# Kernel tuning notes

Hardware: AMD Instinct MI355X
Metric: run time of the kernel (lower is better)

Reference implementation:

```python
import jax, jax.numpy as jnp
import numpy as np
from jax import lax

B, LATENT, HC, COND_OUT, H, INPUT = 64, 512, 1024, 512, 1024, 389
S, SEQ = 16, 512
NOTES = SEQ // S  # 32 notes per subsequence
NL = 2


def _lstm_cell(x, h, c, Wih, Whh, bih, bhh):
    # PyTorch LSTM cell, gate order i, f, g, o
    g = x @ Wih.T + h @ Whh.T + bih + bhh
    i, f, gg, o = jnp.split(g, 4, axis=-1)
    c_new = jax.nn.sigmoid(f) * c + jax.nn.sigmoid(i) * jnp.tanh(gg)
    h_new = jax.nn.sigmoid(o) * jnp.tanh(c_new)
    return h_new, c_new


def setup_inputs() -> dict:
    key = jax.random.key(0)
    ks = iter(jax.random.split(key, 32))
    s = 0.03  # ~ PyTorch LSTM uniform(-1/sqrt(H), 1/sqrt(H)) scale
    def W(shape):
        return jax.random.normal(next(ks), shape, jnp.float32) * s
    return {
        "latent": jax.random.normal(next(ks), (B, LATENT), jnp.float32),
        "target": jax.random.randint(next(ks), (B, SEQ), 0, INPUT),
        "teacher_forcing": 0,
        "h0_dec": jax.random.normal(next(ks), (S, NL, B, H), jnp.float32),
        "c0_dec": jax.random.normal(next(ks), (S, NL, B, H), jnp.float32),
        # conductor LSTM (2 layers)
        "Wih_c0": W((4 * HC, LATENT)), "Whh_c0": W((4 * HC, HC)),
        "bih_c0": W((4 * HC,)), "bhh_c0": W((4 * HC,)),
        "Wih_c1": W((4 * HC, HC)), "Whh_c1": W((4 * HC, HC)),
        "bih_c1": W((4 * HC,)), "bhh_c1": W((4 * HC,)),
        # conductor output projection
        "Wco": W((COND_OUT, HC)), "bco": W((COND_OUT,)),
        # decoder LSTM (2 layers); input = concat(prev_note, emb) -> INPUT+COND_OUT
        "Wih_d0": W((4 * H, INPUT + COND_OUT)), "Whh_d0": W((4 * H, H)),
        "bih_d0": W((4 * H,)), "bhh_d0": W((4 * H,)),
        "Wih_d1": W((4 * H, H)), "Whh_d1": W((4 * H, H)),
        "bih_d1": W((4 * H,)), "bhh_d1": W((4 * H,)),
        # decoder output projection
        "Wdo": W((INPUT, H)), "bdo": W((INPUT,)),
    }


def reference(latent, target, teacher_forcing, h0_dec, c0_dec,
              Wih_c0, Whh_c0, bih_c0, bhh_c0, Wih_c1, Whh_c1, bih_c1, bhh_c1,
              Wco, bco,
              Wih_d0, Whh_d0, bih_d0, bhh_d0, Wih_d1, Whh_d1, bih_d1, bhh_d1,
              Wdo, bdo):
    # use_teacher_forcing is hard-coded False in the source; target is unused.
    del target, teacher_forcing

    def outer(carry, xs):
        hc, cc, prev = carry          # hc, cc: [2,B,HC]; prev: [B,INPUT]
        hd_init, cd_init = xs         # [2,B,H] random decoder init per subsequence
        h0, c0 = _lstm_cell(latent, hc[0], cc[0], Wih_c0, Whh_c0, bih_c0, bhh_c0)
        h1, c1 = _lstm_cell(h0, hc[1], cc[1], Wih_c1, Whh_c1, bih_c1, bhh_c1)
        emb = jnp.tanh(h1 @ Wco.T + bco)  # [B, COND_OUT]

        def inner(ic, _):
            p, hdi, cdi = ic
            x = jnp.concatenate([p, emb], axis=-1)  # [B, INPUT+COND_OUT]
            hd0, cd0 = _lstm_cell(x, hdi[0], cdi[0], Wih_d0, Whh_d0, bih_d0, bhh_d0)
            hd1, cd1 = _lstm_cell(hd0, hdi[1], cdi[1], Wih_d1, Whh_d1, bih_d1, bhh_d1)
            note = jnp.tanh(hd1 @ Wdo.T + bdo)  # [B, INPUT]
            return (note, jnp.stack([hd0, hd1]), jnp.stack([cd0, cd1])), note

        (prev_new, _, _), notes = lax.scan(inner, (prev, hd_init, cd_init), None, length=NOTES)
        return (jnp.stack([h0, h1]), jnp.stack([c0, c1]), prev_new), notes

    init = (jnp.zeros((NL, B, HC), jnp.float32),
            jnp.zeros((NL, B, HC), jnp.float32),
            jnp.zeros((B, INPUT), jnp.float32))
    _, out = lax.scan(outer, init, (h0_dec, c0_dec))
    # out: [S, NOTES, B, INPUT] -> [B, SEQ, INPUT]
    return out.transpose(2, 0, 1, 3).reshape(B, SEQ, INPUT)
```

## Files before the change

### kernel.cpp

```cpp
#include <hip/hip_runtime.h>
#include <hip/hip_bf16.h>

typedef unsigned int  u32;
typedef unsigned short u16;
typedef __attribute__((ext_vector_type(8))) short short8;
typedef __attribute__((ext_vector_type(4))) float f32x4;
typedef __attribute__((ext_vector_type(4))) unsigned int u32x4;
typedef __attribute__((ext_vector_type(2))) unsigned int u32x2;

#define MFMA(a,b,c) __builtin_amdgcn_mfma_f32_16x16x32_bf16(a,b,c,0,0,0)

#define NWG    256
#define KD0    1448
#define KD1    2056
#define KPROJ  1032

#define WS_ARR   0
#define WS_DONE  1024
#define WS_SEM   1536
#define SEM_HD0  0
#define SEM_HD1  1
#define SEM_NOTE 2
#define SEM_I0   3
#define SEM_I1   4

#define WS_NOTE  4096
#define WS_HD0   (WS_NOTE + 2*52*64*8*2)
#define WS_HD1   (WS_HD0 + 2*128*64*8*2)
#define WS_HC0   (WS_HD1 + 2*128*64*8*2)
#define WS_HC1   (WS_HC0 + 2*128*64*8*2)
#define WS_EMB   (WS_HC1 + 2*128*64*8*2)
#define WS_LAT   (WS_EMB + 15*64*64*8*2)
#define WS_END   (WS_EMB + 16*64*64*8*2)

#define NOTE_PAR 26624
#define HD_PAR   65536
#define HC_PAR   65536
#define EMB_S    32768

#define L_GSC   0
#define L_GC0X  8448
#define L_CC0   12800
#define L_CC1   13824
#define L_BC1   14848
#define L_PACK  14912
#define L_ROLE  16960
#define L_WD0   L_ROLE
#define L_G0E   (L_ROLE + 32*KD0*2)
#define L_CST0  (L_G0E + 8448)
#define L_BD0   (L_CST0 + 2048)
#define L_WPJ   (L_BD0 + 128)
#define L_BPJ   (L_WPJ + 16*KPROJ*2)
#define L_WD1   L_ROLE
#define L_CST1  (L_ROLE + 32*KD1*2)
#define L_BD1   (L_CST1 + 2048)
#define LDS_BYTES 153600

__device__ __forceinline__ u16 f2bf(float f){
  u32 u = __float_as_uint(f);
  u32 r = (u + 0x7FFFu + ((u >> 16) & 1u)) >> 16;
  return (u16)r;
}
__device__ __forceinline__ float sigm(float x){ return 1.f/(1.f + __expf(-x)); }
__device__ __forceinline__ float tanh_(float x){
  float e = __expf(-2.f*fabsf(x));
  float t = (1.f - e)/(1.f + e);
  return x < 0.f ? -t : t;
}
__device__ __forceinline__ short8 ldw8(const float* p0){
  short8 r;
#pragma unroll
  for (int j = 0; j < 8; ++j) r[j] = (short)f2bf(p0[j]);
  return r;
}

__device__ __forceinline__ void gst1(u32* p, u32 v){
  asm volatile("global_store_dword %0, %1, off sc1" :: "v"(p), "v"(v) : "memory");
}
__device__ __forceinline__ void gst4(u16* p, u32x4 v){
  asm volatile("global_store_dwordx4 %0, %1, off sc1" :: "v"(p), "v"(v) : "memory");
}
__device__ __forceinline__ u32 ld1_sc1(const u32* p){
  u32 v;
  asm volatile("global_load_dword %0, %1, off sc1\n\ts_waitcnt vmcnt(0)"
               : "=v"(v) : "v"(p) : "memory");
  return v;
}

#define AISSUE(dst, addr) \
  asm volatile("global_load_dwordx4 %0, %1, off sc1" : "=&v"(dst) : "v"(addr) : "memory")
#define AWAITN(cnt) do{ \
  asm volatile("s_waitcnt vmcnt(" #cnt ")" ::: "memory"); \
  __builtin_amdgcn_sched_barrier(0x3F7); }while(0)

template<int NA, int NB, bool TWO>
__device__ __forceinline__ void mm_lds(
    const u16* Wl, int ldw16, const u16* xal, const u16* xbl,
    f32x4& a0, f32x4& a1)
{
  constexpr int N = NA + NB;
  constexpr int R = (N < 32) ? N : 32;
  short8 ab[R];
#define XADDR(i) (((i) < NA) ? (xal + (size_t)(i)*2048) : (xbl + (size_t)((i)-NA)*2048))
#define ACONS(i) { \
    a0 = MFMA(ab[(i) % R], *(const short8*)(Wl + (size_t)(i)*32), a0); \
    if constexpr (TWO) a1 = MFMA(ab[(i) % R], *(const short8*)(Wl + ldw16 + (size_t)(i)*32), a1); }
  if constexpr (N <= 32){
#pragma unroll
    for (int i = 0; i < N; ++i) AISSUE(ab[i], XADDR(i));
    AWAITN(0);
#pragma unroll
    for (int i = 0; i < N; ++i) ACONS(i);
  } else {
#pragma unroll
    for (int i = 0; i < 32; ++i) AISSUE(ab[i], XADDR(i));
#pragma unroll
    for (int i = 0; i < N - 32; ++i){
      AWAITN(31);
      ACONS(i);
      AISSUE(ab[i & 31], XADDR(i + 32));
    }
    AWAITN(0);
#pragma unroll
    for (int i = N - 32; i < N; ++i) ACONS(i);
  }
#undef ACONS
#undef XADDR
}

template<int NA, int NB, bool TWO>
__device__ __forceinline__ void mm_gw(
    const float* w00, const float* w01, const float* w10, const float* w11,
    const u16* xal, const u16* xbl, f32x4& a0, f32x4& a1)
{
  constexpr int N = NA + NB;
  static_assert((N % 16) == 0, "");
  short8 ab[16];
#define XADDR(i) (((i) < NA) ? (xal + (size_t)(i)*2048) : (xbl + (size_t)((i)-NA)*2048))
#pragma unroll
  for (int b = 0; b < N/16; ++b){
#pragma unroll
    for (int j = 0; j < 16; ++j) AISSUE(ab[j], XADDR(b*16 + j));
    AWAITN(0);
#pragma unroll
    for (int j = 0; j < 16; ++j){
      const int i = b*16 + j;
      const float* wp0 = (i < NA) ? (w00 + (size_t)i*32) : (w01 + (size_t)(i-NA)*32);
      a0 = MFMA(ab[j], ldw8(wp0), a0);
      if constexpr (TWO){
        const float* wp1 = (i < NA) ? (w10 + (size_t)i*32) : (w11 + (size_t)(i-NA)*32);
        a1 = MFMA(ab[j], ldw8(wp1), a1);
      }
    }
  }
#undef XADDR
}

__device__ __forceinline__ void sem_post_lane(char* ws, int sem, int wg){
  asm volatile("s_waitcnt vmcnt(0)" ::: "memory");
  if (threadIdx.x == 0){
    u32* c = (u32*)(ws + WS_SEM + sem*512 + (wg & 7)*64);
    __hip_atomic_fetch_add(c, 1u, __ATOMIC_RELAXED, __HIP_MEMORY_SCOPE_AGENT);
  }
}
__device__ __forceinline__ void sem_wait(char* ws, int sem, u32 target){
  if (threadIdx.x < 64){
    const int l = threadIdx.x;
    const u32* c = (const u32*)(ws + WS_SEM + sem*512 + l*64);
    for (;;){
      u32 v = (l < 8) ? ld1_sc1(c) : 0u;
#pragma unroll
      for (int off = 32; off; off >>= 1)
        v += (u32)__shfl_xor((int)v, off, 64);
      if (v >= target) break;
      __builtin_amdgcn_s_sleep(1);
    }
  }
  __syncthreads();
}

__device__ __forceinline__ void gbar(char* ws, int grp, int mem, u32 ep){
  u32* arr  = (u32*)(ws + WS_ARR) + grp*32;
  u32* done = (u32*)(ws + WS_DONE);
  asm volatile("s_waitcnt vmcnt(0)" ::: "memory");
  __syncthreads();
  if (threadIdx.x < 64){
    const int l = threadIdx.x;
    if (l == 0) gst1(&arr[mem], ep);
    if (mem == 0){
      for (;;){
        u32 m = (l < 32) ? ld1_sc1(&arr[l]) : ep;
#pragma unroll
        for (int off = 32; off; off >>= 1){
          u32 o = (u32)__shfl_xor((int)m, off, 64);
          m = o < m ? o : m;
        }
        if (m >= ep) break;
      }
      if (l == 0) gst1(&done[grp], ep);
    }
    for (;;){
      u32 m = (l < 8) ? ld1_sc1(&done[l]) : ep;
#pragma unroll
      for (int off = 32; off; off >>= 1){
        u32 o = (u32)__shfl_xor((int)m, off, 64);
        m = o < m ? o : m;
      }
      if (m >= ep) break;
      __builtin_amdgcn_s_sleep(1);
    }
  }
  __syncthreads();
}

struct Params {
  const float *latent, *h0_dec, *c0_dec;
  const float *Wih_c0, *Whh_c0, *bih_c0, *bhh_c0;
  const float *Wih_c1, *Whh_c1, *bih_c1, *bhh_c1;
  const float *Wco, *bco;
  const float *Wih_d0, *Whh_d0, *bih_d0, *bhh_d0;
  const float *Wih_d1, *Whh_d1, *bih_d1, *bhh_d1;
  const float *Wdo, *bdo;
  float* out;
  char* ws;
};

__device__ __forceinline__ void cell_pw(
    const float* g_sc, const float* gadd, const float* bias,
    float* cst, u32* pack, int tid)
{
  const int b = tid & 63, k = tid >> 6;
  u32 hp = 0;
#pragma unroll
  for (int j = 0; j < 2; ++j){
    const int u = 2*k + j;
    float gi = g_sc[b*33 + u];
    float gf = g_sc[b*33 + 8 + u];
    float gg = g_sc[b*33 + 16 + u];
    float go = g_sc[b*33 + 24 + u];
    if (gadd){
      gi += gadd[b*33 + u];      gf += gadd[b*33 + 8 + u];
      gg += gadd[b*33 + 16 + u]; go += gadd[b*33 + 24 + u];
    }
    if (bias){
      gi += bias[u]; gf += bias[8 + u]; gg += bias[16 + u]; go += bias[24 + u];
    }
    float c = sigm(gf)*cst[u*64 + b] + sigm(gi)*tanh_(gg);
    const float h = sigm(go)*tanh_(c);
    cst[u*64 + b] = c;
    hp |= ((u32)f2bf(h)) << (16*j);
  }
  pack[b*4 + k] = hp;
}

__device__ __forceinline__ void cond_pw(
    f32x4 acc, const float* gadd17, const float* bias16,
    float* cstL, u16* pack16, int lane, int wid)
{
  const int r = lane & 15, q = lane >> 4, m0 = wid*16;
  float v[4], vf[4], vg[4], vo[4];
#pragma unroll
  for (int i = 0; i < 4; ++i){
    const int brow = m0 + q*4 + i;
    float x = acc[i];
    if (gadd17) x += gadd17[brow*17 + r];
    if (bias16) x += bias16[r];
    v[i] = x;
  }
#pragma unroll
  for (int i = 0; i < 4; ++i){
    vf[i] = __shfl_xor(v[i], 4, 64);
    vg[i] = __shfl_xor(v[i], 8, 64);
    vo[i] = __shfl_xor(v[i], 12, 64);
  }
  if (r < 4){
#pragma unroll
    for (int i = 0; i < 4; ++i){
      const int brow = m0 + q*4 + i;
      float c = sigm(vf[i])*cstL[r*64 + brow] + sigm(v[i])*tanh_(vg[i]);
      const float h = sigm(vo[i])*tanh_(c);
      cstL[r*64 + brow] = c;
      pack16[brow*4 + r] = f2bf(h);
    }
  }
}

__global__ void init_kernel(const float* latent, char* ws){
  const int i = blockIdx.x*blockDim.x + threadIdx.x;
  if (i < 1024) ((u32*)ws)[i] = 0u;
  if (i < 26624) ((u32*)(ws + WS_NOTE))[i] = 0u;
  if (i < 65536){ ((u32*)(ws + WS_HC0))[i] = 0u; ((u32*)(ws + WS_HC1))[i] = 0u; }
  if (i < 32768){
    const int b = i >> 9, k = i & 511;
    ((u16*)(ws + WS_LAT))[((size_t)(k >> 3)*64 + b)*8 + (k & 7)] = f2bf(latent[i]);
  }
}

__global__ void __launch_bounds__(256, 1) decoder_kernel(Params P){
  extern __shared__ char smem[];
  const int wg = blockIdx.x, tid = threadIdx.x;
  const int lane = tid & 63, wid = tid >> 6;
  const int rr = lane & 15, q = lane >> 4, m0 = wid*16;
  const int grp = wg >> 5, mem = wg & 31;

  u16* noteb = (u16*)(P.ws + WS_NOTE);
  u16* hd0b  = (u16*)(P.ws + WS_HD0);
  u16* hd1b  = (u16*)(P.ws + WS_HD1);
  u16* hc0b  = (u16*)(P.ws + WS_HC0);
  u16* hc1b  = (u16*)(P.ws + WS_HC1);
  u16* embA  = (u16*)(P.ws + WS_EMB);
  const u16* latg = (const u16*)(P.ws + WS_LAT);

  float* g_sc  = (float*)(smem + L_GSC);
  float* g_c0x = (float*)(smem + L_GC0X);
  float* cc0   = (float*)(smem + L_CC0);
  float* cc1   = (float*)(smem + L_CC1);
  float* bc1   = (float*)(smem + L_BC1);
  u16*   pack16 = (u16*)(smem + L_PACK);
  u32*   packU32 = (u32*)(smem + L_PACK);
  u16*   Wd0  = (u16*)(smem + L_WD0);
  float* g0e  = (float*)(smem + L_G0E);
  float* cst0 = (float*)(smem + L_CST0);
  float* bd0  = (float*)(smem + L_BD0);
  u16*   Wpj  = (u16*)(smem + L_WPJ);
  float* bpj  = (float*)(smem + L_BPJ);
  u16*   Wd1  = (u16*)(smem + L_WD1);
  float* cst1 = (float*)(smem + L_CST1);
  float* bd1  = (float*)(smem + L_BD1);

  const bool is_d0 = (wg < 128);
  const int lofs = (q*64 + m0 + rr)*8;

  if (is_d0){
    for (int r = wid; r < 32; r += 4){
      const int grow = ((r >> 3) << 10) + 8*wg + (r & 7);
      const float* wih = P.Wih_d0 + (size_t)grow*901;
      const float* whh = P.Whh_d0 + (size_t)grow*1024;
      u16* dst = Wd0 + (size_t)r*KD0;
      for (int c = lane; c < 416; c += 64) dst[c] = (c < 389) ? f2bf(wih[c]) : (u16)0;
      for (int c = lane; c < 1024; c += 64) dst[416 + c] = f2bf(whh[c]);
    }
    if (tid < 32){
      const int grow = ((tid >> 3) << 10) + 8*wg + (tid & 7);
      bd0[tid] = P.bih_d0[grow] + P.bhh_d0[grow];
    }
    if (wg < 25){
      for (int r = wid; r < 16; r += 4){
        const int row = 16*wg + r;
        u16* dst = Wpj + (size_t)r*KPROJ;
        if (row < 389){
          const float* w = P.Wdo + (size_t)row*1024;
          for (int c = lane; c < 1024; c += 64) dst[c] = f2bf(w[c]);
        } else {
          for (int c = lane; c < 1024; c += 64) dst[c] = 0;
        }
      }
      if (tid < 16){
        const int row = 16*wg + tid;
        bpj[tid] = (row < 389) ? P.bdo[row] : 0.f;
      }
    }
  } else {
    const int wl = wg - 128;
    for (int r = wid; r < 32; r += 4){
      const int grow = ((r >> 3) << 10) + 8*wl + (r & 7);
      const float* wih = P.Wih_d1 + (size_t)grow*1024;
      const float* whh = P.Whh_d1 + (size_t)grow*1024;
      u16* dst = Wd1 + (size_t)r*KD1;
      for (int c = lane; c < 1024; c += 64) dst[c] = f2bf(wih[c]);
      for (int c = lane; c < 1024; c += 64) dst[1024 + c] = f2bf(whh[c]);
    }
    if (tid < 32){
      const int grow = ((tid >> 3) << 10) + 8*wl + (tid & 7);
      bd1[tid] = P.bih_d1[grow] + P.bhh_d1[grow];
    }
  }
  if (tid < 256){ cc0[tid] = 0.f; cc1[tid] = 0.f; }
  if (tid < 16){
    const int grow = ((tid >> 2) << 10) + 4*wg + (tid & 3);
    bc1[tid] = P.bih_c1[grow] + P.bhh_c1[grow];
  }
  {
    const int grow = ((rr >> 2) << 10) + 4*wg + (rr & 3);
    f32x4 acc = {0.f,0.f,0.f,0.f}, dummy;
    mm_gw<16,0,false>(P.Wih_c0 + (size_t)grow*512 + q*8, nullptr, nullptr, nullptr,
                      latg + lofs, latg + lofs, acc, dummy);
    const float bias = P.bih_c0[grow] + P.bhh_c0[grow];
#pragma unroll
    for (int i = 0; i < 4; ++i)
      g_c0x[(m0 + q*4 + i)*17 + rr] = acc[i] + bias;
  }
  __syncthreads();

  u32 ep = 0;
#define GBAR() gbar(P.ws, grp, mem, ++ep)

  for (int s = 0; s < 16; ++s){
    const int pc = s & 1;
    const u16* hc0_p = hc0b + (size_t)pc*HC_PAR;
    u16*       hc0_n = hc0b + (size_t)(pc ^ 1)*HC_PAR;
    const u16* hc1_p = hc1b + (size_t)pc*HC_PAR;
    u16*       hc1_n = hc1b + (size_t)(pc ^ 1)*HC_PAR;
    const int grow = ((rr >> 2) << 10) + 4*wg + (rr & 3);

    {
      f32x4 acc = {0.f,0.f,0.f,0.f}, dummy;
      mm_gw<32,0,false>(P.Whh_c0 + (size_t)grow*1024 + q*8, nullptr, nullptr, nullptr,
                        hc0_p + lofs, hc0_p + lofs, acc, dummy);
      cond_pw(acc, g_c0x, nullptr, cc0, pack16, lane, wid);
    }
    __syncthreads();
    if (tid < 64){
      u32x2 v = *(const u32x2*)&packU32[tid*2];
      asm volatile("global_store_dwordx2 %0, %1, off sc1"
                   :: "v"(hc0_n + ((size_t)(wg >> 1)*64 + tid)*8 + (wg & 1)*4), "v"(v) : "memory");
    }
    GBAR();

    {
      f32x4 acc = {0.f,0.f,0.f,0.f}, dummy;
      mm_gw<32,32,false>(P.Wih_c1 + (size_t)grow*1024 + q*8,
                         P.Whh_c1 + (size_t)grow*1024 + q*8, nullptr, nullptr,
                         hc0_n + lofs, hc1_p + lofs, acc, dummy);
      cond_pw(acc, nullptr, bc1, cc1, pack16, lane, wid);
    }
    __syncthreads();
    if (tid < 64){
      u32x2 v = *(const u32x2*)&packU32[tid*2];
      asm volatile("global_store_dwordx2 %0, %1, off sc1"
                   :: "v"(hc1_n + ((size_t)(wg >> 1)*64 + tid)*8 + (wg & 1)*4), "v"(v) : "memory");
    }
    GBAR();

    if (wg < 32){
      const int row = 16*wg + rr;
      f32x4 acc = {0.f,0.f,0.f,0.f}, dummy;
      mm_gw<32,0,false>(P.Wco + (size_t)row*1024 + q*8, nullptr, nullptr, nullptr,
                        hc1_n + lofs, hc1_n + lofs, acc, dummy);
      const float bias = P.bco[row];
#pragma unroll
      for (int i = 0; i < 4; ++i)
        pack16[(m0 + q*4 + i)*16 + rr] = f2bf(tanh_(acc[i] + bias));
      __syncthreads();
      if (tid < 64){
        u16* ea = embA + (size_t)s*EMB_S;
        u32x4 v0 = *(const u32x4*)&packU32[tid*8];
        u32x4 v1 = *(const u32x4*)&packU32[tid*8 + 4];
        gst4(ea + ((size_t)(2*wg)*64 + tid)*8, v0);
        gst4(ea + ((size_t)(2*wg + 1)*64 + tid)*8, v1);
      }
    }
    GBAR();
  }

  for (int s = 0; s < 16; ++s){
    const u32 n0 = (u32)s*32u;
    f32x4 sh0 = {0.f,0.f,0.f,0.f}, sh1 = sh0;
    f32x4 t10 = sh0, t11 = sh0;

    sem_wait(P.ws, SEM_NOTE, 25u*n0);

    if (is_d0){
      {
        const int b = tid & 63, k = tid >> 6;
        const size_t src = ((size_t)(s*2 + 0)*64 + b)*1024 + 8*wg + 2*k;
        cst0[(2*k)*64 + b]     = P.c0_dec[src];
        cst0[(2*k + 1)*64 + b] = P.c0_dec[src + 1];
        packU32[b*4 + k] = (u32)f2bf(P.h0_dec[src]) | ((u32)f2bf(P.h0_dec[src + 1]) << 16);
      }
      __syncthreads();
      if (tid < 64){
        u32x4 v = *(const u32x4*)&packU32[tid*4];
        gst4(hd0b + ((size_t)wg*64 + tid)*8, v);
        sem_post_lane(P.ws, SEM_I0, wg);
      }
      {
        const int g0 = ((rr >> 3) << 10) + 8*wg + (rr & 7);
        const int g1 = (((rr + 16) >> 3) << 10) + 8*wg + (rr & 7);
        f32x4 a0 = {0.f,0.f,0.f,0.f}, a1 = {0.f,0.f,0.f,0.f};
        const u16* ea = embA + (size_t)s*EMB_S;
        mm_gw<16,0,true>(P.Wih_d0 + (size_t)g0*901 + 389 + q*8, nullptr,
                         P.Wih_d0 + (size_t)g1*901 + 389 + q*8, nullptr,
                         ea + lofs, ea + lofs, a0, a1);
#pragma unroll
        for (int i = 0; i < 4; ++i){
          g0e[(m0 + q*4 + i)*33 + rr]      = a0[i] + bd0[rr];
          g0e[(m0 + q*4 + i)*33 + 16 + rr] = a1[i] + bd0[rr + 16];
        }
      }
      __syncthreads();
    } else {
      const int wl = wg - 128;
      const int b = tid & 63, k = tid >> 6;
      const size_t src = ((size_t)(s*2 + 1)*64 + b)*1024 + 8*wl + 2*k;
      cst1[(2*k)*64 + b]     = P.c0_dec[src];
      cst1[(2*k + 1)*64 + b] = P.c0_dec[src + 1];
      packU32[b*4 + k] = (u32)f2bf(P.h0_dec[src]) | ((u32)f2bf(P.h0_dec[src + 1]) << 16);
      __syncthreads();
      if (tid < 64){
        u32x4 v = *(const u32x4*)&packU32[tid*4];
        gst4(hd1b + ((size_t)wl*64 + tid)*8, v);
        sem_post_lane(P.ws, SEM_I1, wg);
      }
    }

    for (int t = 0; t < 32; ++t){
      const u32 n = n0 + (u32)t;
      const int p = t & 1;
      const u16* note_p = noteb + (size_t)p*NOTE_PAR;
      u16*       note_n = noteb + (size_t)(p ^ 1)*NOTE_PAR;
      const u16* hd0_p = hd0b + (size_t)p*HD_PAR;
      u16*       hd0_n = hd0b + (size_t)(p ^ 1)*HD_PAR;
      const u16* hd1_p = hd1b + (size_t)p*HD_PAR;
      u16*       hd1_n = hd1b + (size_t)(p ^ 1)*HD_PAR;

      if (is_d0){
        if (t == 0) sem_wait(P.ws, SEM_I0, 128u*(u32)(s + 1));
        else        sem_wait(P.ws, SEM_NOTE, 25u*n);

        f32x4 a0, a1;
        if (t == 0){
          a0 = (f32x4){0.f,0.f,0.f,0.f}; a1 = a0;
          mm_lds<13,32,true>(Wd0 + (size_t)rr*KD0 + q*8, 16*KD0,
                             note_p + lofs, hd0_p + lofs, a0, a1);
        } else {
          a0 = sh0; a1 = sh1;
          mm_lds<13,0,true>(Wd0 + (size_t)rr*KD0 + q*8, 16*KD0,
                            note_p + lofs, note_p + lofs, a0, a1);
        }
#pragma unroll
        for (int i = 0; i < 4; ++i){
          g_sc[(m0 + q*4 + i)*33 + rr]      = a0[i];
          g_sc[(m0 + q*4 + i)*33 + 16 + rr] = a1[i];
        }
        __syncthreads();
        cell_pw(g_sc, g0e, nullptr, cst0, packU32, tid);
        __syncthreads();
        if (tid < 64){
          u32x4 v = *(const u32x4*)&packU32[tid*4];
          gst4(hd0_n + ((size_t)wg*64 + tid)*8, v);
          sem_post_lane(P.ws, SEM_HD0, wg);
        }

        if (t < 31){
          sem_wait(P.ws, SEM_HD0, 128u*(n + 1u));
          sh0 = (f32x4){0.f,0.f,0.f,0.f}; sh1 = sh0;
          mm_lds<32,0,true>(Wd0 + (size_t)rr*KD0 + 416 + q*8, 16*KD0,
                            hd0_n + lofs, hd0_n + lofs, sh0, sh1);
        }

        if (wg < 25){
          sem_wait(P.ws, SEM_HD1, 128u*(n + 1u));
          f32x4 b0 = {0.f,0.f,0.f,0.f}, b1;
          mm_lds<32,0,false>(Wpj + (size_t)rr*KPROJ + q*8, 0,
                             hd1_n + lofs, hd1_n + lofs, b0, b1);
          const int row = 16*wg + rr;
          const int seq = s*32 + t;
          const float bias = bpj[rr];
#pragma unroll
          for (int i = 0; i < 4; ++i){
            const int brow = m0 + q*4 + i;
            const float nv = tanh_(b0[i] + bias);
            if (row < 389) P.out[((size_t)brow*512 + seq)*389 + row] = nv;
            pack16[brow*16 + rr] = f2bf(nv);
          }
          __syncthreads();
          if (tid < 64){
            u32x4 v0 = *(const u32x4*)&packU32[tid*8];
            u32x4 v1 = *(const u32x4*)&packU32[tid*8 + 4];
            gst4(note_n + ((size_t)(2*wg)*64 + tid)*8, v0);
            gst4(note_n + ((size_t)(2*wg + 1)*64 + tid)*8, v1);
            sem_post_lane(P.ws, SEM_NOTE, wg);
          }
        }
      } else {
        sem_wait(P.ws, SEM_HD0, 128u*(n + 1u));
        if (t == 0) sem_wait(P.ws, SEM_I1, 128u*(u32)(s + 1));

        f32x4 a0, a1;
        if (t == 0){
          a0 = (f32x4){0.f,0.f,0.f,0.f}; a1 = a0;
          mm_lds<32,32,true>(Wd1 + (size_t)rr*KD1 + q*8, 16*KD1,
                             hd0_n + lofs, hd1_p + lofs, a0, a1);
        } else {
          a0 = t10; a1 = t11;
          mm_lds<32,0,true>(Wd1 + (size_t)rr*KD1 + q*8, 16*KD1,
                            hd0_n + lofs, hd0_n + lofs, a0, a1);
        }
#pragma unroll
        for (int i = 0; i < 4; ++i){
          g_sc[(m0 + q*4 + i)*33 + rr]      = a0[i];
          g_sc[(m0 + q*4 + i)*33 + 16 + rr] = a1[i];
        }
        __syncthreads();
        cell_pw(g_sc, nullptr, bd1, cst1, packU32, tid);
        __syncthreads();
        if (tid < 64){
          u32x4 v = *(const u32x4*)&packU32[tid*4];
          gst4(hd1_n + ((size_t)(wg - 128)*64 + tid)*8, v);
          sem_post_lane(P.ws, SEM_HD1, wg);
        }

        if (t < 31){
          sem_wait(P.ws, SEM_HD1, 128u*(n + 1u));
          t10 = (f32x4){0.f,0.f,0.f,0.f}; t11 = t10;
          mm_lds<32,0,true>(Wd1 + (size_t)rr*KD1 + 1024 + q*8, 16*KD1,
                            hd1_n + lofs, hd1_n + lofs, t10, t11);
        }
      }
    }
  }
#undef GBAR
}

extern "C" void kernel_launch(void* const* d_in, const int* in_sizes, int n_in,
                              void* d_out, int out_size, void* d_ws, size_t ws_size,
                              hipStream_t stream){
  (void)in_sizes; (void)n_in; (void)out_size;
  if (ws_size < (size_t)WS_END) return;

  Params P;
  P.latent = (const float*)d_in[0];
  P.h0_dec = (const float*)d_in[3];
  P.c0_dec = (const float*)d_in[4];
  P.Wih_c0 = (const float*)d_in[5];  P.Whh_c0 = (const float*)d_in[6];
  P.bih_c0 = (const float*)d_in[7];  P.bhh_c0 = (const float*)d_in[8];
  P.Wih_c1 = (const float*)d_in[9];  P.Whh_c1 = (const float*)d_in[10];
  P.bih_c1 = (const float*)d_in[11]; P.bhh_c1 = (const float*)d_in[12];
  P.Wco    = (const float*)d_in[13]; P.bco    = (const float*)d_in[14];
  P.Wih_d0 = (const float*)d_in[15]; P.Whh_d0 = (const float*)d_in[16];
  P.bih_d0 = (const float*)d_in[17]; P.bhh_d0 = (const float*)d_in[18];
  P.Wih_d1 = (const float*)d_in[19]; P.Whh_d1 = (const float*)d_in[20];
  P.bih_d1 = (const float*)d_in[21]; P.bhh_d1 = (const float*)d_in[22];
  P.Wdo    = (const float*)d_in[23]; P.bdo    = (const float*)d_in[24];
  P.out = (float*)d_out;
  P.ws  = (char*)d_ws;

  hipLaunchKernelGGL(init_kernel, dim3(256), dim3(256), 0, stream,
                     (const float*)d_in[0], (char*)d_ws);

  hipFuncSetAttribute(reinterpret_cast<const void*>(&decoder_kernel),
                      hipFuncAttributeMaxDynamicSharedMemorySize, LDS_BYTES);
  hipLaunchKernelGGL(decoder_kernel, dim3(NWG), dim3(256), LDS_BYTES, stream, P);
}
```

Before: 9.752 ms.

## Use per-step ring buffers for recurrent state so activation loads can use cached path

Replaces the ping-pong double buffers for note, hd0 and hd1 with a buffer per time step (32 slots plus init slots), so each address is written only once within a subsequence. This lets the activation loads in the LDS-weight matmul drop the sc1 cache-bypass bit and use normal cached global loads. An acquire fence and block barrier are added after the per-subsequence note wait to keep visibility correct. It costs more workspace, and it risks reading stale lines if cross-workgroup coherence is not maintained across subsequences.

```diff
diff --git a/kernel.cpp b/kernel.cpp
--- a/kernel.cpp
+++ b/kernel.cpp
@@ -24,19 +24,20 @@
 #define SEM_I0   3
 #define SEM_I1   4
 
+#define NOTE_SZ  26624
+#define HD_SZ    65536
+#define EMB_S    32768
+
 #define WS_NOTE  4096
-#define WS_HD0   (WS_NOTE + 2*52*64*8*2)
-#define WS_HD1   (WS_HD0 + 2*128*64*8*2)
-#define WS_HC0   (WS_HD1 + 2*128*64*8*2)
-#define WS_HC1   (WS_HC0 + 2*128*64*8*2)
-#define WS_EMB   (WS_HC1 + 2*128*64*8*2)
-#define WS_LAT   (WS_EMB + 15*64*64*8*2)
-#define WS_END   (WS_EMB + 16*64*64*8*2)
-
-#define NOTE_PAR 26624
-#define HD_PAR   65536
+#define WS_HD0   (WS_NOTE + 32*NOTE_SZ*2)
+#define WS_HD1   (WS_HD0 + 33*HD_SZ*2)
+#define WS_HC0   (WS_HD1 + 33*HD_SZ*2)
+#define WS_HC1   (WS_HC0 + 2*HD_SZ*2)
+#define WS_EMB   (WS_HC1 + 2*HD_SZ*2)
+#define WS_LAT   (WS_EMB + 15*EMB_S*2)
+#define WS_END   (WS_EMB + 16*EMB_S*2)
+
 #define HC_PAR   65536
-#define EMB_S    32768
 
 #define L_GSC   0
 #define L_GC0X  8448
@@ -89,6 +90,8 @@
 
 #define AISSUE(dst, addr) \
   asm volatile("global_load_dwordx4 %0, %1, off sc1" : "=&v"(dst) : "v"(addr) : "memory")
+#define AISSUE_C(dst, addr) \
+  asm volatile("global_load_dwordx4 %0, %1, off" : "=&v"(dst) : "v"(addr) : "memory")
 #define AWAITN(cnt) do{ \
   asm volatile("s_waitcnt vmcnt(" #cnt ")" ::: "memory"); \
   __builtin_amdgcn_sched_barrier(0x3F7); }while(0)
@@ -107,18 +110,18 @@
     if constexpr (TWO) a1 = MFMA(ab[(i) % R], *(const short8*)(Wl + ldw16 + (size_t)(i)*32), a1); }
   if constexpr (N <= 32){
 #pragma unroll
-    for (int i = 0; i < N; ++i) AISSUE(ab[i], XADDR(i));
+    for (int i = 0; i < N; ++i) AISSUE_C(ab[i], XADDR(i));
     AWAITN(0);
 #pragma unroll
     for (int i = 0; i < N; ++i) ACONS(i);
   } else {
 #pragma unroll
-    for (int i = 0; i < 32; ++i) AISSUE(ab[i], XADDR(i));
+    for (int i = 0; i < 32; ++i) AISSUE_C(ab[i], XADDR(i));
 #pragma unroll
     for (int i = 0; i < N - 32; ++i){
       AWAITN(31);
       ACONS(i);
-      AISSUE(ab[i & 31], XADDR(i + 32));
+      AISSUE_C(ab[i & 31], XADDR(i + 32));
     }
     AWAITN(0);
 #pragma unroll
@@ -288,7 +291,7 @@
 __global__ void init_kernel(const float* latent, char* ws){
   const int i = blockIdx.x*blockDim.x + threadIdx.x;
   if (i < 1024) ((u32*)ws)[i] = 0u;
-  if (i < 26624) ((u32*)(ws + WS_NOTE))[i] = 0u;
+  if (i < 13312) ((u32*)(ws + WS_NOTE + 31*NOTE_SZ*2))[i] = 0u;
   if (i < 65536){ ((u32*)(ws + WS_HC0))[i] = 0u; ((u32*)(ws + WS_HC1))[i] = 0u; }
   if (i < 32768){
     const int b = i >> 9, k = i & 511;
@@ -304,12 +307,14 @@
   const int grp = wg >> 5, mem = wg & 31;
 
   u16* noteb = (u16*)(P.ws + WS_NOTE);
-  u16* hd0b  = (u16*)(P.ws + WS_HD0);
-  u16* hd1b  = (u16*)(P.ws + WS_HD1);
+  u16* hd0R  = (u16*)(P.ws + WS_HD0);
+  u16* hd1R  = (u16*)(P.ws + WS_HD1);
   u16* hc0b  = (u16*)(P.ws + WS_HC0);
   u16* hc1b  = (u16*)(P.ws + WS_HC1);
   u16* embA  = (u16*)(P.ws + WS_EMB);
   const u16* latg = (const u16*)(P.ws + WS_LAT);
+  u16* hd0_init = hd0R + (size_t)32*HD_SZ;
+  u16* hd1_init = hd1R + (size_t)32*HD_SZ;
 
   float* g_sc  = (float*)(smem + L_GSC);
   float* g_c0x = (float*)(smem + L_GC0X);
@@ -459,6 +464,8 @@
     f32x4 t10 = sh0, t11 = sh0;
 
     sem_wait(P.ws, SEM_NOTE, 25u*n0);
+    __builtin_amdgcn_fence(__ATOMIC_ACQUIRE, "agent");
+    __syncthreads();
 
     if (is_d0){
       {
@@ -471,7 +478,7 @@
       __syncthreads();
       if (tid < 64){
         u32x4 v = *(const u32x4*)&packU32[tid*4];
-        gst4(hd0b + ((size_t)wg*64 + tid)*8, v);
+        gst4(hd0_init + ((size_t)wg*64 + tid)*8, v);
         sem_post_lane(P.ws, SEM_I0, wg);
       }
       {
@@ -499,20 +506,17 @@
       __syncthreads();
       if (tid < 64){
         u32x4 v = *(const u32x4*)&packU32[tid*4];
-        gst4(hd1b + ((size_t)wl*64 + tid)*8, v);
+        gst4(hd1_init + ((size_t)wl*64 + tid)*8, v);
         sem_post_lane(P.ws, SEM_I1, wg);
       }
     }
 
     for (int t = 0; t < 32; ++t){
       const u32 n = n0 + (u32)t;
-      const int p = t & 1;
-      const u16* note_p = noteb + (size_t)p*NOTE_PAR;
-      u16*       note_n = noteb + (size_t)(p ^ 1)*NOTE_PAR;
-      const u16* hd0_p = hd0b + (size_t)p*HD_PAR;
-      u16*       hd0_n = hd0b + (size_t)(p ^ 1)*HD_PAR;
-      const u16* hd1_p = hd1b + (size_t)p*HD_PAR;
-      u16*       hd1_n = hd1b + (size_t)(p ^ 1)*HD_PAR;
+      const u16* note_r = noteb + (size_t)((t + 31) & 31)*NOTE_SZ;
+      u16*       note_w = noteb + (size_t)t*NOTE_SZ;
+      u16* hd0_t = hd0R + (size_t)t*HD_SZ;
+      u16* hd1_t = hd1R + (size_t)t*HD_SZ;
 
       if (is_d0){
         if (t == 0) sem_wait(P.ws, SEM_I0, 128u*(u32)(s + 1));
@@ -522,11 +526,11 @@
         if (t == 0){
           a0 = (f32x4){0.f,0.f,0.f,0.f}; a1 = a0;
           mm_lds<13,32,true>(Wd0 + (size_t)rr*KD0 + q*8, 16*KD0,
-                             note_p + lofs, hd0_p + lofs, a0, a1);
+                             note_r + lofs, hd0_init + lofs, a0, a1);
         } else {
           a0 = sh0; a1 = sh1;
           mm_lds<13,0,true>(Wd0 + (size_t)rr*KD0 + q*8, 16*KD0,
-                            note_p + lofs, note_p + lofs, a0, a1);
+                            note_r + lofs, note_r + lofs, a0, a1);
         }
 #pragma unroll
         for (int i = 0; i < 4; ++i){
@@ -538,7 +542,7 @@
         __syncthreads();
         if (tid < 64){
           u32x4 v = *(const u32x4*)&packU32[tid*4];
-          gst4(hd0_n + ((size_t)wg*64 + tid)*8, v);
+          gst4(hd0_t + ((size_t)wg*64 + tid)*8, v);
           sem_post_lane(P.ws, SEM_HD0, wg);
         }
 
@@ -546,14 +550,14 @@
           sem_wait(P.ws, SEM_HD0, 128u*(n + 1u));
           sh0 = (f32x4){0.f,0.f,0.f,0.f}; sh1 = sh0;
           mm_lds<32,0,true>(Wd0 + (size_t)rr*KD0 + 416 + q*8, 16*KD0,
-                            hd0_n + lofs, hd0_n + lofs, sh0, sh1);
+                            hd0_t + lofs, hd0_t + lofs, sh0, sh1);
         }
 
         if (wg < 25){
           sem_wait(P.ws, SEM_HD1, 128u*(n + 1u));
           f32x4 b0 = {0.f,0.f,0.f,0.f}, b1;
           mm_lds<32,0,false>(Wpj + (size_t)rr*KPROJ + q*8, 0,
-                             hd1_n + lofs, hd1_n + lofs, b0, b1);
+                             hd1_t + lofs, hd1_t + lofs, b0, b1);
           const int row = 16*wg + rr;
           const int seq = s*32 + t;
           const float bias = bpj[rr];
@@ -568,8 +572,8 @@
           if (tid < 64){
             u32x4 v0 = *(const u32x4*)&packU32[tid*8];
             u32x4 v1 = *(const u32x4*)&packU32[tid*8 + 4];
-            gst4(note_n + ((size_t)(2*wg)*64 + tid)*8, v0);
-            gst4(note_n + ((size_t)(2*wg + 1)*64 + tid)*8, v1);
+            gst4(note_w + ((size_t)(2*wg)*64 + tid)*8, v0);
+            gst4(note_w + ((size_t)(2*wg + 1)*64 + tid)*8, v1);
             sem_post_lane(P.ws, SEM_NOTE, wg);
           }
         }
@@ -581,11 +585,11 @@
         if (t == 0){
           a0 = (f32x4){0.f,0.f,0.f,0.f}; a1 = a0;
           mm_lds<32,32,true>(Wd1 + (size_t)rr*KD1 + q*8, 16*KD1,
-                             hd0_n + lofs, hd1_p + lofs, a0, a1);
+                             hd0_t + lofs, hd1_init + lofs, a0, a1);
         } else {
           a0 = t10; a1 = t11;
           mm_lds<32,0,true>(Wd1 + (size_t)rr*KD1 + q*8, 16*KD1,
-                            hd0_n + lofs, hd0_n + lofs, a0, a1);
+                            hd0_t + lofs, hd0_t + lofs, a0, a1);
         }
 #pragma unroll
         for (int i = 0; i < 4; ++i){
@@ -597,7 +601,7 @@
         __syncthreads();
         if (tid < 64){
           u32x4 v = *(const u32x4*)&packU32[tid*4];
-          gst4(hd1_n + ((size_t)(wg - 128)*64 + tid)*8, v);
+          gst4(hd1_t + ((size_t)(wg - 128)*64 + tid)*8, v);
           sem_post_lane(P.ws, SEM_HD1, wg);
         }
 
@@ -605,7 +609,7 @@
           sem_wait(P.ws, SEM_HD1, 128u*(n + 1u));
           t10 = (f32x4){0.f,0.f,0.f,0.f}; t11 = t10;
           mm_lds<32,0,true>(Wd1 + (size_t)rr*KD1 + 1024 + q*8, 16*KD1,
-                            hd1_n + lofs, hd1_n + lofs, t10, t11);
+                            hd1_t + lofs, hd1_t + lofs, t10, t11);
         }
       }
     }
```

Result: no change. 9.877 ms (+1.3%).
